# Kernel tuning notes

Measured on AMD Instinct MI355X. Metric: run time of the kernel, lower is better.

## Reference

```python
import jax, jax.numpy as jnp
import numpy as np

TEMPERATURE = 0.5
NEG_FILL = -9e15


def setup_inputs() -> dict:
    key = jax.random.key(0)
    k1, k2 = jax.random.split(key)
    B, D = 8192, 128
    z1 = jax.random.normal(k1, (B, D), dtype=jnp.float32)
    z2 = jax.random.normal(k2, (B, D), dtype=jnp.float32)
    return {"z1": z1, "z2": z2}


def reference(z1, z2):
    B = z1.shape[0]
    N = 2 * B
    z = jnp.concatenate([z1, z2], axis=0)              # [N, D]
    sim = jnp.matmul(z, z.T) / TEMPERATURE             # [N, N]
    eye = jnp.eye(N, dtype=bool)
    sim = jnp.where(eye, NEG_FILL, sim)
    idx = jnp.arange(N)
    pos_idx = (idx + B) % N
    positives = sim[idx, pos_idx]                      # [N]
    loss = -positives + jax.scipy.special.logsumexp(sim, axis=1)
    return loss.mean()
```

## Files before the change

kernel.cpp:

```cpp
#include <hip/hip_runtime.h>
#include <stdint.h>


typedef __attribute__((ext_vector_type(4)))  int   i32x4;
typedef __attribute__((ext_vector_type(16))) int   i32x16;

#define N_TOT   16384
#define NHALF   8192
#define NQ      16
#define QW      (N_TOT / NQ)
#define BN      64
#define NT      (QW / BN)
#define BM      256
#define NRB     (N_TOT / BM)
#define CSH     128.0f
#define LN2     0.69314718055994530942f
#define QS      27.178299f

__device__ __forceinline__ void gload_lds16(const void* g, void* l) {
    __builtin_amdgcn_global_load_lds(
        (const __attribute__((address_space(1))) void*)g,
        (__attribute__((address_space(3))) void*)l, 16, 0, 0);
}

__device__ __forceinline__ unsigned pack4(float4 f) {
    int q0 = (int)rintf(fminf(fmaxf(f.x * QS, -127.f), 127.f));
    int q1 = (int)rintf(fminf(fmaxf(f.y * QS, -127.f), 127.f));
    int q2 = (int)rintf(fminf(fmaxf(f.z * QS, -127.f), 127.f));
    int q3 = (int)rintf(fminf(fmaxf(f.w * QS, -127.f), 127.f));
    return (unsigned)(q0 & 255) | ((unsigned)(q1 & 255) << 8) |
           ((unsigned)(q2 & 255) << 16) | ((unsigned)q3 << 24);
}

__global__ __launch_bounds__(256) void k_castpos(const float* __restrict__ z1,
                                                 const float* __restrict__ z2,
                                                 unsigned* __restrict__ zb,
                                                 float* __restrict__ pos_part,
                                                 float* __restrict__ ws_acc) {
    __shared__ float red[4];
    int i = blockIdx.x * 256 + threadIdx.x;
    if (i == 0) { ws_acc[0] = 0.f; ((unsigned int*)ws_acc)[1] = 0u; }
    float4 a = ((const float4*)z1)[i];
    float4 b = ((const float4*)z2)[i];
    zb[i]          = pack4(a);
    zb[i + 262144] = pack4(b);
    float s = a.x * b.x + a.y * b.y + a.z * b.z + a.w * b.w;
    for (int o = 32; o; o >>= 1) s += __shfl_xor(s, o);
    int lane = threadIdx.x & 63, w = threadIdx.x >> 6;
    if (lane == 0) red[w] = s;
    __syncthreads();
    if (threadIdx.x == 0) pos_part[blockIdx.x] = red[0] + red[1] + red[2] + red[3];
}

#define MFMA_SUB(TB, SDX, O0, O1) do {                                        \
    const int c_ = (SDX) * 32 + l31;                                          \
    O0 = kZ16; O1 = kZ16;                                                     \
    _Pragma("unroll")                                                         \
    for (int m_ = 0; m_ < 4; ++m_) {                                          \
        i32x4 a_ = *(const i32x4*)((TB) + (m_ * 2 + h) * 1024 + c_ * 16);     \
        O0 = __builtin_amdgcn_mfma_i32_32x32x32_i8(a_, rf0[m_], O0, 0, 0, 0); \
        O1 = __builtin_amdgcn_mfma_i32_32x32x32_i8(a_, rf1[m_], O1, 0, 0, 0); \
    } } while (0)

#define EXP_SUB(X0, X1, CB) do {                                              \
    if ((CB) == rowB) {                                                       \
        _Pragma("unroll")                                                     \
        for (int r2_ = 0; r2_ < 16; ++r2_) {                                  \
            int crow_ = (r2_ & 3) + 8 * (r2_ >> 2) + 4 * h;                   \
            if (crow_ == l31) X0[r2_] = -(1 << 30);                           \
        } }                                                                   \
    if ((CB) == rowB + 32) {                                                  \
        _Pragma("unroll")                                                     \
        for (int r2_ = 0; r2_ < 16; ++r2_) {                                  \
            int crow_ = (r2_ & 3) + 8 * (r2_ >> 2) + 4 * h;                   \
            if (crow_ == l31) X1[r2_] = -(1 << 30);                           \
        } }                                                                   \
    _Pragma("unroll")                                                         \
    for (int r2_ = 0; r2_ < 16; ++r2_) {                                      \
        float x0_ = fmaf((float)X0[r2_], 0.00390625f, -CSH);                  \
        float x1_ = fmaf((float)X1[r2_], 0.00390625f, -CSH);                  \
        sa[r2_ & 3] += __builtin_amdgcn_exp2f(x0_);                           \
        sb[r2_ & 3] += __builtin_amdgcn_exp2f(x1_);                           \
    } } while (0)

__global__ __launch_bounds__(256) void k_main(const unsigned* __restrict__ zbu,
                                              float* __restrict__ ps) {
    __shared__ char tile[2][8192];
    const char* zb8 = (const char*)zbu;

    const int tid  = threadIdx.x;
    const int lane = tid & 63;
    const int w    = tid >> 6;
    const int h    = lane >> 5;
    const int l31  = lane & 31;

    const int bid = blockIdx.x;
    const int q   = bid >> 6;
    const int rb  = bid & 63;
    const int rowB     = rb * BM + w * 64;
    const int colStart = q * QW;

    i32x4 rf0[4], rf1[4];
    #pragma unroll
    for (int m = 0; m < 4; ++m) {
        rf0[m] = *(const i32x4*)(zb8 + (size_t)(rowB + l31) * 128 + m * 32 + h * 16);
        rf1[m] = *(const i32x4*)(zb8 + (size_t)(rowB + 32 + l31) * 128 + m * 32 + h * 16);
    }

    int gsoff[2];
    #pragma unroll
    for (int j = 0; j < 2; ++j) gsoff[j] = lane * 128 + (w * 2 + j) * 16;

    #pragma unroll
    for (int j = 0; j < 2; ++j)
        gload_lds16(zb8 + (size_t)colStart * 128 + gsoff[j],
                    &tile[0][0] + (w * 2 + j) * 1024);
    #pragma unroll
    for (int j = 0; j < 2; ++j)
        gload_lds16(zb8 + (size_t)(colStart + BN) * 128 + gsoff[j],
                    &tile[1][0] + (w * 2 + j) * 1024);

    const i32x16 kZ16 = {};
    float sa[4] = {0.f, 0.f, 0.f, 0.f};
    float sb[4] = {0.f, 0.f, 0.f, 0.f};
    i32x16 A0, A1;

    for (int t = 0; t < NT; ++t) {
        if (t < NT - 1) asm volatile("s_waitcnt vmcnt(2)" ::: "memory");
        else            asm volatile("s_waitcnt vmcnt(0)" ::: "memory");
        __builtin_amdgcn_s_barrier();
        const char* tb = &tile[t & 1][0];
        const int cb0 = colStart + t * BN;
        MFMA_SUB(tb, 0, A0, A1);
        EXP_SUB(A0, A1, cb0);
        MFMA_SUB(tb, 1, A0, A1);
        EXP_SUB(A0, A1, cb0 + 32);
        __builtin_amdgcn_s_barrier();
        if (t + 2 < NT) {
            #pragma unroll
            for (int j = 0; j < 2; ++j)
                gload_lds16(zb8 + (size_t)(colStart + (t + 2) * BN) * 128 + gsoff[j],
                            &tile[t & 1][0] + (w * 2 + j) * 1024);
        }
    }

    float sA = (sa[0] + sa[1]) + (sa[2] + sa[3]);
    float sB = (sb[0] + sb[1]) + (sb[2] + sb[3]);
    sA += __shfl_xor(sA, 32);
    sB += __shfl_xor(sB, 32);
    if (lane < 32) {
        ps[(size_t)q * N_TOT + rowB + l31]      = sA;
        ps[(size_t)q * N_TOT + rowB + 32 + l31] = sB;
    }
}

__global__ __launch_bounds__(256) void k_cf(const float* __restrict__ ps,
                                            const float* __restrict__ pos_part,
                                            float* __restrict__ ws_acc,
                                            float* __restrict__ out) {
    __shared__ float red[4];
    __shared__ int last;
    const int tid = threadIdx.x;
    const int base = blockIdx.x * 1024;
    float ls = 0.f;
    #pragma unroll
    for (int k = 0; k < 4; ++k) {
        int row = base + k * 256 + tid;
        float s = 0.f;
        #pragma unroll
        for (int qq = 0; qq < NQ; ++qq) s += ps[(size_t)qq * N_TOT + row];
        ls += LN2 * (CSH + log2f(s));
    }
    for (int o = 32; o; o >>= 1) ls += __shfl_xor(ls, o);
    int lane = tid & 63, wv = tid >> 6;
    if (lane == 0) red[wv] = ls;
    __syncthreads();
    if (tid == 0) {
        atomicAdd(&ws_acc[0], red[0] + red[1] + red[2] + red[3]);
        __threadfence();
        unsigned int old = atomicAdd(&((unsigned int*)ws_acc)[1], 1u);
        last = (old == 15u) ? 1 : 0;
    }
    __syncthreads();
    if (last) {
        float p = pos_part[tid] + pos_part[tid + 256] +
                  pos_part[tid + 512] + pos_part[tid + 768];
        for (int o = 32; o; o >>= 1) p += __shfl_xor(p, o);
        if (lane == 0) red[wv] = p;
        __syncthreads();
        if (tid == 0) {
            float lse_tot = atomicAdd(&ws_acc[0], 0.f);
            float pos_tot = red[0] + red[1] + red[2] + red[3];
            out[0] = (lse_tot - 4.0f * pos_tot) * (1.0f / (float)N_TOT);
        }
    }
}

extern "C" void kernel_launch(void* const* d_in, const int* in_sizes, int n_in,
                              void* d_out, int out_size, void* d_ws, size_t ws_size,
                              hipStream_t stream) {
    const float* z1 = (const float*)d_in[0];
    const float* z2 = (const float*)d_in[1];
    float* out = (float*)d_out;

    char* ws = (char*)d_ws;
    float* ps       = (float*)ws;
    float* ws_acc   = (float*)(ws + (1u << 20));
    float* pos_part = (float*)(ws + (1u << 20) + 1024);
    unsigned* zb    = (unsigned*)(ws + (2u << 20));

    k_castpos<<<dim3(1024), dim3(256), 0, stream>>>(z1, z2, zb, pos_part, ws_acc);
    k_main<<<dim3(NRB * NQ), dim3(256), 0, stream>>>(zb, ps);
    k_cf<<<dim3(16), dim3(256), 0, stream>>>(ps, pos_part, ws_acc, out);
}
```

Measured before the change: 127.9 us.

## Software-pipeline exp accumulation of previous sub-tile with current MFMAs

Splits the per-sub-tile work into MFMA, mask and exp phases, then software-pipelines them. The exp2 accumulation of the previous 32-column sub-tile is interleaved with the int8 MFMAs of the current one, using ping-pong accumulators (A/P), and the last sub-tile is drained after the loop. The aim is to hide transcendental and VALU latency behind matrix-core work. The cost is 32 extra live VGPRs per lane, and the first iteration runs exp over zero-initialised registers, which adds negligible 2^-128 terms.

```diff
diff --git a/kernel.cpp b/kernel.cpp
--- a/kernel.cpp
+++ b/kernel.cpp
@@ -52,7 +52,12 @@
     if (threadIdx.x == 0) pos_part[blockIdx.x] = red[0] + red[1] + red[2] + red[3];
 }
 
-#define MFMA_SUB(TB, SDX, O0, O1) do {                                        \
+#define EXP1(V, C) do {                                                       \
+    float x_ = fmaf((float)(V), 0.00390625f, -CSH);                           \
+    C += __builtin_amdgcn_exp2f(x_);                                          \
+} while (0)
+
+#define FUSED_SUB(TB, SDX, O0, O1, E0, E1) do {                               \
     const int c_ = (SDX) * 32 + l31;                                          \
     O0 = kZ16; O1 = kZ16;                                                     \
     _Pragma("unroll")                                                         \
@@ -60,9 +65,17 @@
         i32x4 a_ = *(const i32x4*)((TB) + (m_ * 2 + h) * 1024 + c_ * 16);     \
         O0 = __builtin_amdgcn_mfma_i32_32x32x32_i8(a_, rf0[m_], O0, 0, 0, 0); \
         O1 = __builtin_amdgcn_mfma_i32_32x32x32_i8(a_, rf1[m_], O1, 0, 0, 0); \
+        EXP1(E0[4 * m_ + 0], sa[0]);                                          \
+        EXP1(E0[4 * m_ + 1], sa[1]);                                          \
+        EXP1(E0[4 * m_ + 2], sa[2]);                                          \
+        EXP1(E0[4 * m_ + 3], sa[3]);                                          \
+        EXP1(E1[4 * m_ + 0], sb[0]);                                          \
+        EXP1(E1[4 * m_ + 1], sb[1]);                                          \
+        EXP1(E1[4 * m_ + 2], sb[2]);                                          \
+        EXP1(E1[4 * m_ + 3], sb[3]);                                          \
     } } while (0)
 
-#define EXP_SUB(X0, X1, CB) do {                                              \
+#define MASK_SUB(X0, X1, CB) do {                                             \
     if ((CB) == rowB) {                                                       \
         _Pragma("unroll")                                                     \
         for (int r2_ = 0; r2_ < 16; ++r2_) {                                  \
@@ -75,12 +88,13 @@
             int crow_ = (r2_ & 3) + 8 * (r2_ >> 2) + 4 * h;                   \
             if (crow_ == l31) X1[r2_] = -(1 << 30);                           \
         } }                                                                   \
+} while (0)
+
+#define EXP_DRAIN(X0, X1) do {                                                \
     _Pragma("unroll")                                                         \
     for (int r2_ = 0; r2_ < 16; ++r2_) {                                      \
-        float x0_ = fmaf((float)X0[r2_], 0.00390625f, -CSH);                  \
-        float x1_ = fmaf((float)X1[r2_], 0.00390625f, -CSH);                  \
-        sa[r2_ & 3] += __builtin_amdgcn_exp2f(x0_);                           \
-        sb[r2_ & 3] += __builtin_amdgcn_exp2f(x1_);                           \
+        EXP1(X0[r2_], sa[r2_ & 3]);                                           \
+        EXP1(X1[r2_], sb[r2_ & 3]);                                           \
     } } while (0)
 
 __global__ __launch_bounds__(256) void k_main(const unsigned* __restrict__ zbu,
@@ -123,7 +137,7 @@
     const i32x16 kZ16 = {};
     float sa[4] = {0.f, 0.f, 0.f, 0.f};
     float sb[4] = {0.f, 0.f, 0.f, 0.f};
-    i32x16 A0, A1;
+    i32x16 A0, A1, P0 = kZ16, P1 = kZ16;
 
     for (int t = 0; t < NT; ++t) {
         if (t < NT - 1) asm volatile("s_waitcnt vmcnt(2)" ::: "memory");
@@ -131,10 +145,10 @@
         __builtin_amdgcn_s_barrier();
         const char* tb = &tile[t & 1][0];
         const int cb0 = colStart + t * BN;
-        MFMA_SUB(tb, 0, A0, A1);
-        EXP_SUB(A0, A1, cb0);
-        MFMA_SUB(tb, 1, A0, A1);
-        EXP_SUB(A0, A1, cb0 + 32);
+        FUSED_SUB(tb, 0, A0, A1, P0, P1);
+        MASK_SUB(A0, A1, cb0);
+        FUSED_SUB(tb, 1, P0, P1, A0, A1);
+        MASK_SUB(P0, P1, cb0 + 32);
         __builtin_amdgcn_s_barrier();
         if (t + 2 < NT) {
             #pragma unroll
@@ -143,6 +157,7 @@
                             &tile[t & 1][0] + (w * 2 + j) * 1024);
         }
     }
+    EXP_DRAIN(P0, P1);
 
     float sA = (sa[0] + sa[1]) + (sa[2] + sa[3]);
     float sB = (sb[0] + sb[1]) + (sb[2] + sb[3]);
```

New measurement: 126.2 us. About the same (-1.4%).
